# Kernel optimization log

Measured on AMD Instinct MI355X. Metric: run time of the kernel, lower is better.

The kernel has to match this reference:

```python
import jax, jax.numpy as jnp
from jax import lax
import numpy as np

NH = 4                      # num_heads in CrossScaleCom
KS = [3, 5, 7, 9]           # per-head depthwise kernel sizes
WS = 2                      # window_size in LocalFeatureGuided
GGM_K = 7                   # guide-token generator kernel size


def _dwconv(x, w, stride, pad):
    # depthwise conv: w has shape (C, 1, k, k), feature_group_count = C
    return lax.conv_general_dilated(
        x, w, (stride, stride), [(pad, pad), (pad, pad)],
        feature_group_count=x.shape[1],
        dimension_numbers=("NCHW", "OIHW", "NCHW"))


def _forward(x, dw_w0, dw_b0, dw_w1, dw_b1, dw_w2, dw_b2, dw_w3, dw_b3,
             csc_w, csc_b, bn_gamma, bn_beta, bn_mean, bn_var,
             ggm_w, ggm_b, qkv_w, qkv_b, proj_w, proj_b):
    B, C, H, W = x.shape
    cph = C // NH
    # ---- CrossScaleCom: per-head multi-scale depthwise convs ----
    xh = x.reshape(B, NH, cph, H, W)
    dws = [(dw_w0, dw_b0), (dw_w1, dw_b1), (dw_w2, dw_b2), (dw_w3, dw_b3)]
    heads = [_dwconv(xh[:, i], w, 1, KS[i] // 2) + b[None, :, None, None]
             for i, (w, b) in enumerate(dws)]
    y = jnp.stack(heads, 1)                      # (B, NH, cph, H, W)
    y = y.transpose(0, 2, 1, 3, 4).reshape(B, C, H, W)  # channel shuffle
    y = jnp.einsum("bchw,oc->bohw", y, csc_w) + csc_b[None, :, None, None]
    Co = y.shape[1]
    # ---- LocalFeatureGuided ----
    # ggm: BatchNorm (eval) -> GELU (exact) -> depthwise conv k=7 stride=WS
    inv = bn_gamma / jnp.sqrt(bn_var + 1e-5)
    g = (y - bn_mean[None, :, None, None]) * inv[None, :, None, None] \
        + bn_beta[None, :, None, None]
    g = jax.nn.gelu(g, approximate=False)
    g = _dwconv(g, ggm_w, WS, GGM_K // 2) + ggm_b[None, :, None, None]  # (B,Co,Ho,Wo)
    Ho, Wo = H // WS, W // WS
    L = Ho * Wo
    # unfold(kernel=WS, stride=WS) -> (B, Co, WS*WS, L), torch unfold ordering
    xu = y.reshape(B, Co, Ho, WS, Wo, WS).transpose(0, 1, 3, 5, 2, 4)
    xu = xu.reshape(B, Co, WS * WS, L)
    tokens = jnp.concatenate([g.reshape(B, Co, 1, L), xu], axis=2)  # (B,Co,5,L)
    # 1x1 conv over channel dim == einsum
    qkv = jnp.einsum("bcpl,oc->bopl", tokens, qkv_w) + qkv_b[None, :, None, None]
    q, k, v = jnp.split(qkv, 3, axis=1)          # each (B, Co, 5, L)
    # tiny 5x5 attention per (batch, channel), contracting over windows L
    attn = jnp.einsum("bcpl,bcql->bcpq", q, k) / (Co ** 0.5)
    attn = jax.nn.softmax(attn, axis=-1)
    out = jnp.einsum("bcpq,bcql->bcpl", attn, v)  # (B, Co, 5, L)
    out = out[:, :, 0, :].reshape(B, Co, Ho, Wo)  # guide-token output
    out = jnp.einsum("bchw,oc->bohw", out, proj_w) + proj_b[None, :, None, None]
    return out


def setup_inputs() -> dict:
    key = jax.random.key(0)
    ks = jax.random.split(key, 16)
    B, Cin, Cout, H, W = 8, 64, 128, 224, 224
    cph = Cin // NH
    s = 0.05
    d = {"x": jax.random.normal(ks[0], (B, Cin, H, W), jnp.float32)}
    for i, kk in enumerate(KS):
        d[f"dw_w{i}"] = jax.random.normal(ks[1 + i], (cph, 1, kk, kk), jnp.float32) * s
        d[f"dw_b{i}"] = jnp.zeros((cph,), jnp.float32)
    d["csc_w"] = jax.random.normal(ks[5], (Cout, Cin), jnp.float32) * s
    d["csc_b"] = jnp.zeros((Cout,), jnp.float32)
    d["bn_gamma"] = jnp.ones((Cout,), jnp.float32)
    d["bn_beta"] = jnp.zeros((Cout,), jnp.float32)
    d["bn_mean"] = jnp.zeros((Cout,), jnp.float32)
    d["bn_var"] = jnp.ones((Cout,), jnp.float32)
    d["ggm_w"] = jax.random.normal(ks[6], (Cout, 1, GGM_K, GGM_K), jnp.float32) * s
    d["ggm_b"] = jnp.zeros((Cout,), jnp.float32)
    d["qkv_w"] = jax.random.normal(ks[7], (3 * Cout, Cout), jnp.float32) * s
    d["qkv_b"] = jnp.zeros((3 * Cout,), jnp.float32)
    d["proj_w"] = jax.random.normal(ks[8], (Cout, Cout), jnp.float32) * s
    d["proj_b"] = jnp.zeros((Cout,), jnp.float32)
    return d


def reference(x, dw_w0, dw_b0, dw_w1, dw_b1, dw_w2, dw_b2, dw_w3, dw_b3,
              csc_w, csc_b, bn_gamma, bn_beta, bn_mean, bn_var,
              ggm_w, ggm_b, qkv_w, qkv_b, proj_w, proj_b):
    return _forward(x, dw_w0, dw_b0, dw_w1, dw_b1, dw_w2, dw_b2, dw_w3, dw_b3,
                    csc_w, csc_b, bn_gamma, bn_beta, bn_mean, bn_var,
                    ggm_w, ggm_b, qkv_w, qkv_b, proj_w, proj_b)
```

## Files before the change

### kernel.cpp

```cpp
#include <hip/hip_runtime.h>

#define BB 8
#define CIN 64
#define CO 128
#define Hdim 224
#define Wdim 224
#define HWt (224*224)
#define HO 112
#define WO 112
#define Lt (112*112)

typedef unsigned short u16;
typedef short bf16x8 __attribute__((ext_vector_type(8)));
typedef float f32x4  __attribute__((ext_vector_type(4)));
#define MFMA16(a,b,c) __builtin_amdgcn_mfma_f32_16x16x32_bf16((a),(b),(c),0,0,0)

__device__ inline u16 f2bf(float f) {
    union { float f; unsigned u; } v; v.f = f;
    unsigned r = (v.u + 0x7fffu + ((v.u >> 16) & 1u)) >> 16;
    return (u16)r;
}
__device__ inline float bf2f(u16 h) {
    union { unsigned u; float f; } v; v.u = ((unsigned)h) << 16; return v.f;
}
__device__ inline float uasf(unsigned u) {
    union { unsigned u; float f; } v; v.u = u; return v.f;
}
__device__ inline float sum8bf(uint4 v) {
    return bf2f(v.x & 0xffff) + bf2f(v.x >> 16) + bf2f(v.y & 0xffff) + bf2f(v.y >> 16)
         + bf2f(v.z & 0xffff) + bf2f(v.z >> 16) + bf2f(v.w & 0xffff) + bf2f(v.w >> 16);
}

__device__ inline float gelu_fast(float x) {
    float z  = x * 0.7071067811865476f;
    float az = fabsf(z);
    float t  = __builtin_amdgcn_rcpf(fmaf(0.3275911f, az, 1.0f));
    float p  = fmaf(fmaf(fmaf(fmaf(1.061405429f, t, -1.453152027f), t,
                    1.421413741f), t, -0.284496736f), t, 0.254829592f);
    float e  = __expf(-z * z);
    float er = copysignf(1.0f - p * t * e, z);
    return 0.5f * x * (1.0f + er);
}

__global__ void zero_kernel(float* __restrict__ p, int n4) {
    int i = blockIdx.x * 256 + threadIdx.x;
    if (i < n4) ((float4*)p)[i] = make_float4(0.f, 0.f, 0.f, 0.f);
}

template<int HEAD>
__global__ __launch_bounds__(256) void dw_conv(
    const float* __restrict__ x, const float* __restrict__ w,
    const float* __restrict__ bias, u16* __restrict__ dwb)
{
    constexpr int K   = 3 + 2*HEAD;
    constexpr int PAD = HEAD + 1;
    constexpr int R   = 32 + 2*PAD;
    const int tile = blockIdx.x;
    const int c    = blockIdx.y;
    const int b    = blockIdx.z;
    const int th = (tile/7)*32, tw = (tile%7)*32;
    __shared__ float patch[R*40];
    const int tid = threadIdx.x;
    const float* xin = x + (size_t)(b*CIN + HEAD*16 + c)*HWt;
    for (int idx = tid; idx < R*40; idx += 256) {
        int r = idx / 40, cc = idx - r*40;
        int gy = th - PAD + r, gx = tw - 4 + cc;
        float v = 0.f;
        if (gy >= 0 && gy < Hdim && gx >= 0 && gx < Wdim) v = xin[gy*Wdim + gx];
        patch[idx] = v;
    }
    float wreg[K*K];
    const float* wp = w + c*K*K;
    #pragma unroll
    for (int i = 0; i < K*K; i++) wreg[i] = wp[i];
    const float bv = bias[c];
    __syncthreads();

    const int ty = tid >> 3, x0 = (tid & 7) * 4;
    float acc[4] = {bv, bv, bv, bv};
    #pragma unroll
    for (int ky = 0; ky < K; ky++) {
        float rr[12];
        *(float4*)&rr[0] = *(const float4*)&patch[(ty+ky)*40 + x0];
        *(float4*)&rr[4] = *(const float4*)&patch[(ty+ky)*40 + x0 + 4];
        *(float4*)&rr[8] = *(const float4*)&patch[(ty+ky)*40 + x0 + 8];
        #pragma unroll
        for (int kx = 0; kx < K; kx++) {
            const float wv = wreg[ky*K + kx];
            #pragma unroll
            for (int j = 0; j < 4; j++)
                acc[j] = fmaf(rr[j + kx + 4 - PAD], wv, acc[j]);
        }
    }
    const int s = c*4 + HEAD;
    u16 o4[4] = {f2bf(acc[0]), f2bf(acc[1]), f2bf(acc[2]), f2bf(acc[3])};
    *(uint2*)&dwb[(size_t)(b*CIN + s)*HWt + (th+ty)*Wdim + tw + x0] = *(uint2*)o4;
}

__global__ __launch_bounds__(256) void csc_mfma(
    const float* __restrict__ W, const float* __restrict__ bias,
    const u16* __restrict__ dwb, u16* __restrict__ y4)
{
    const int b  = blockIdx.z;
    const int p0 = blockIdx.x * 128;
    __shared__ u16 Abuf[128*72];
    __shared__ u16 Tbuf[32*132];
    const int tid = threadIdx.x;
    const int wv = tid >> 6, ln = tid & 63;
    const int mh = (wv >> 1)*64, nh = (wv & 1)*64;
    const int lm = ln & 15, kq = ln >> 4;
    for (int t = tid; t < 1024; t += 256) {
        int r = t >> 3, kk = (t & 7)*8;
        const float* src = &W[r*64 + kk];
        float4 f0 = *(const float4*)src, f1 = *(const float4*)(src+4);
        u16 tmp[8] = {f2bf(f0.x),f2bf(f0.y),f2bf(f0.z),f2bf(f0.w),
                      f2bf(f1.x),f2bf(f1.y),f2bf(f1.z),f2bf(f1.w)};
        *(uint4*)&Abuf[r*72 + kk] = *(uint4*)tmp;
    }
    const u16* Db = dwb + (size_t)b*CIN*HWt;
    f32x4 acc[4][4];
    #pragma unroll
    for (int i=0;i<4;i++)
        #pragma unroll
        for (int j=0;j<4;j++) acc[i][j] = (f32x4){0.f,0.f,0.f,0.f};

    for (int kc = 0; kc < 64; kc += 32) {
        __syncthreads();
        for (int t = tid; t < 512; t += 256) {
            int k = t >> 4, n0 = (t & 15)*8;
            *(uint4*)&Tbuf[k*132 + n0] = *(const uint4*)&Db[(size_t)(kc+k)*HWt + p0 + n0];
        }
        __syncthreads();
        bf16x8 af[4], bfr[4];
        #pragma unroll
        for (int tm=0;tm<4;tm++)
            af[tm] = *(bf16x8*)&Abuf[(mh + tm*16 + lm)*72 + kc + kq*8];
        #pragma unroll
        for (int tn=0;tn<4;tn++) {
            int n = nh + tn*16 + lm;
            #pragma unroll
            for (int j=0;j<8;j++) bfr[tn][j] = (short)Tbuf[(kq*8+j)*132 + n];
        }
        #pragma unroll
        for (int tm=0;tm<4;tm++)
            #pragma unroll
            for (int tn=0;tn<4;tn++)
                acc[tm][tn] = MFMA16(af[tm], bfr[tn], acc[tm][tn]);
    }
    #pragma unroll
    for (int tm=0;tm<4;tm++) {
        #pragma unroll
        for (int r=0;r<4;r++) {
            int o = mh + tm*16 + kq*4 + r;
            float bb = bias[o];
            #pragma unroll
            for (int tn=0;tn<4;tn++) {
                int p = p0 + nh + tn*16 + lm;
                int gy = p / 224, gx = p - gy*224;
                int w = (gy&1)*2 + (gx&1);
                y4[((size_t)(b*CO + o)*4 + w)*Lt + (gy>>1)*WO + (gx>>1)]
                    = f2bf(acc[tm][tn][r] + bb);
            }
        }
    }
}

__global__ __launch_bounds__(256) void ggm_kernel(const u16* __restrict__ y4,
    const float* __restrict__ gamma, const float* __restrict__ beta,
    const float* __restrict__ mean, const float* __restrict__ var,
    const float* __restrict__ gw, const float* __restrict__ gb,
    u16* __restrict__ gbf)
{
    const int ho0 = blockIdx.x * 16;
    const int c   = blockIdx.y;
    const int b   = blockIdx.z;
    __shared__ float patch[37*272];
    const int tid = threadIdx.x;

    const float inv = gamma[c] * rsqrtf(var[c] + 1e-5f);
    const float bsh = fmaf(-mean[c], inv, beta[c]);
    const u16* ybc = y4 + (size_t)(b*CO + c)*4*Lt;

    for (int idx = tid; idx < 37*14; idx += 256) {
        int r = idx / 14, q = idx - r*14;
        int gy = 2*ho0 - 3 + r;
        float* dst = &patch[r*272 + 4*((r>>1)&7) + 8 + 16*q];
        if (gy >= 0 && gy < Hdim) {
            const u16* pe = ybc + (size_t)((gy&1)*2)*Lt + (gy>>1)*WO + 8*q;
            uint4 ve = *(const uint4*)pe;
            uint4 vo = *(const uint4*)(pe + Lt);
            unsigned eu[4] = {ve.x, ve.y, ve.z, ve.w};
            unsigned ou[4] = {vo.x, vo.y, vo.z, vo.w};
            float o[16];
            #pragma unroll
            for (int i = 0; i < 4; i++) {
                float e0 = uasf(eu[i] << 16), e1 = uasf(eu[i] & 0xffff0000u);
                float d0 = uasf(ou[i] << 16), d1 = uasf(ou[i] & 0xffff0000u);
                o[4*i+0] = gelu_fast(fmaf(e0, inv, bsh));
                o[4*i+1] = gelu_fast(fmaf(d0, inv, bsh));
                o[4*i+2] = gelu_fast(fmaf(e1, inv, bsh));
                o[4*i+3] = gelu_fast(fmaf(d1, inv, bsh));
            }
            #pragma unroll
            for (int i = 0; i < 4; i++)
                *(float4*)&dst[4*i] = *(float4*)&o[4*i];
        } else {
            float4 z = make_float4(0.f,0.f,0.f,0.f);
            #pragma unroll
            for (int i = 0; i < 4; i++) *(float4*)&dst[4*i] = z;
        }
    }
    for (int idx = tid; idx < 37*2; idx += 256) {
        int r = idx >> 1, side = idx & 1;
        float* dst = &patch[r*272 + 4*((r>>1)&7) + (side ? 232 : 0)];
        float4 z = make_float4(0.f,0.f,0.f,0.f);
        *(float4*)&dst[0] = z; *(float4*)&dst[4] = z;
    }
    float wk[49];
    const float* wp = gw + c*49;
    #pragma unroll
    for (int i = 0; i < 49; i++) wk[i] = wp[i];
    const float bv = gb[c];
    __syncthreads();

    const int ty = tid >> 4, m = tid & 15;
    if (m < 14) {
        float acc[8] = {bv,bv,bv,bv,bv,bv,bv,bv};
        #pragma unroll
        for (int ky = 0; ky < 7; ky++) {
            int r = 2*ty + ky;
            const float* row = &patch[r*272 + 4*((r>>1)&7) + 16*m + 4];
            float f[24];
            #pragma unroll
            for (int u = 0; u < 6; u++)
                *(float4*)&f[4*u] = *(const float4*)&row[4*u];
            #pragma unroll
            for (int kx = 0; kx < 7; kx++) {
                const float wv = wk[ky*7 + kx];
                #pragma unroll
                for (int j = 0; j < 8; j++)
                    acc[j] = fmaf(f[2*j + kx + 1], wv, acc[j]);
            }
        }
        u16 o8[8];
        #pragma unroll
        for (int j = 0; j < 8; j++) o8[j] = f2bf(acc[j]);
        *(uint4*)&gbf[(size_t)(b*CO + c)*Lt + (ho0 + ty)*WO + 8*m] = *(uint4*)o8;
    }
}

__global__ __launch_bounds__(256) void G_mfma(
    const u16* __restrict__ gbf, const u16* __restrict__ y4,
    float* __restrict__ G)
{
    const int b = blockIdx.z, p = blockIdx.y, split = blockIdx.x;
    const u16* Ab = gbf + (size_t)b*CO*Lt;
    const u16* Bb; int brs;
    if (p == 0) { Bb = Ab; brs = Lt; }
    else        { Bb = y4 + ((size_t)b*CO*4 + (p-1))*Lt; brs = 4*Lt; }
    __shared__ u16 Abuf[128*40];
    __shared__ u16 Bbuf[128*40];
    const int tid = threadIdx.x;
    const int wv = tid >> 6, ln = tid & 63;
    const int mh = (wv >> 1)*64, nh = (wv & 1)*64;
    const int lm = ln & 15, kq = ln >> 4;
    f32x4 acc[4][4];
    #pragma unroll
    for (int i=0;i<4;i++)
        #pragma unroll
        for (int j=0;j<4;j++) acc[i][j] = (f32x4){0.f,0.f,0.f,0.f};

    for (int ci = split; ci < 392; ci += 32) {
        const int l0 = ci*32;
        __syncthreads();
        for (int t = tid; t < 512; t += 256) {
            int r = t >> 2, kk = (t & 3)*8;
            *(uint4*)&Abuf[r*40 + kk] = *(const uint4*)&Ab[(size_t)r*Lt  + l0 + kk];
            *(uint4*)&Bbuf[r*40 + kk] = *(const uint4*)&Bb[(size_t)r*brs + l0 + kk];
        }
        __syncthreads();
        bf16x8 af[4], bfr[4];
        #pragma unroll
        for (int tm=0;tm<4;tm++)
            af[tm]  = *(bf16x8*)&Abuf[(mh + tm*16 + lm)*40 + kq*8];
        #pragma unroll
        for (int tn=0;tn<4;tn++)
            bfr[tn] = *(bf16x8*)&Bbuf[(nh + tn*16 + lm)*40 + kq*8];
        #pragma unroll
        for (int tm=0;tm<4;tm++)
            #pragma unroll
            for (int tn=0;tn<4;tn++)
                acc[tm][tn] = MFMA16(af[tm], bfr[tn], acc[tm][tn]);
    }
    float* Go = G + ((size_t)(b*5 + p))*CO*CO;
    #pragma unroll
    for (int tm=0;tm<4;tm++)
        #pragma unroll
        for (int r=0;r<4;r++) {
            int mrow = mh + tm*16 + kq*4 + r;
            #pragma unroll
            for (int tn=0;tn<4;tn++)
                atomicAdd(&Go[mrow*CO + nh + tn*16 + lm], acc[tm][tn][r]);
        }
}

__global__ void S_kernel(const u16* __restrict__ gbf, const u16* __restrict__ y4,
                         float* __restrict__ S)
{
    const int b = blockIdx.x >> 7, c = blockIdx.x & 127;
    const u16* gr = gbf + (size_t)(b*CO+c)*Lt;
    const u16* yr = y4  + (size_t)(b*CO+c)*4*Lt;
    float vals[5] = {0.f,0.f,0.f,0.f,0.f};
    for (int i = threadIdx.x*8; i < Lt; i += 256*8)
        vals[0] += sum8bf(*(const uint4*)&gr[i]);
    #pragma unroll
    for (int w=0; w<4; w++)
        for (int i = threadIdx.x*8; i < Lt; i += 256*8)
            vals[1+w] += sum8bf(*(const uint4*)&yr[(size_t)w*Lt + i]);
    #pragma unroll
    for (int off=32; off>0; off>>=1) {
        #pragma unroll
        for (int q=0;q<5;q++) vals[q] += __shfl_down(vals[q], off);
    }
    __shared__ float red[4][5];
    const int wid = threadIdx.x>>6, lane = threadIdx.x&63;
    if (lane==0) {
        #pragma unroll
        for (int q=0;q<5;q++) red[wid][q] = vals[q];
    }
    __syncthreads();
    if (threadIdx.x==0) {
        #pragma unroll
        for (int q=0;q<5;q++)
            S[((size_t)b*5 + q)*CO + c] = red[0][q]+red[1][q]+red[2][q]+red[3][q];
    }
}

__global__ __launch_bounds__(256) void fused_logits_kernel(
    const float* __restrict__ G, const float* __restrict__ S,
    const float* __restrict__ qkv_w, const float* __restrict__ qkv_b,
    float* __restrict__ lg)
{
    const int p = blockIdx.x, b = blockIdx.y;
    __shared__ float Wl[32*132];
    __shared__ float Al[32*132];
    __shared__ float KGl[128*128];
    const int tid = threadIdx.x;
    const int og = (tid >> 4) * 8;
    const int pg = (tid & 15) * 8;
    const float* Gp = G + (size_t)(b*5 + p)*CO*CO;
    float acc[8][8];
    #pragma unroll
    for (int i=0;i<8;i++)
        #pragma unroll
        for (int j=0;j<8;j++) acc[i][j]=0.f;

    for (int kc = 0; kc < 128; kc += 32) {
        __syncthreads();
        for (int t = tid; t < 4096; t += 256) {
            int kk = t & 31, o = t >> 5;
            Wl[kk*132 + o] = Gp[(size_t)o*CO + kc + kk];
            Al[kk*132 + o] = qkv_w[(size_t)(CO + o)*CO + kc + kk];
        }
        __syncthreads();
        #pragma unroll 4
        for (int kk = 0; kk < 32; kk++) {
            float wv[8], av[8];
            *(float4*)&wv[0] = *(const float4*)&Wl[kk*132+og];
            *(float4*)&wv[4] = *(const float4*)&Wl[kk*132+og+4];
            *(float4*)&av[0] = *(const float4*)&Al[kk*132+pg];
            *(float4*)&av[4] = *(const float4*)&Al[kk*132+pg+4];
            #pragma unroll
            for (int i=0;i<8;i++)
                #pragma unroll
                for (int j=0;j<8;j++)
                    acc[i][j] = fmaf(wv[i], av[j], acc[i][j]);
        }
    }
    #pragma unroll
    for (int i=0;i<8;i++) {
        #pragma unroll
        for (int j=0;j<8;j+=4)
            *(float4*)&KGl[(og+i)*128 + pg + j] = *(float4*)&acc[i][j];
    }
    __syncthreads();
    if (tid < 128) {
        const int c = tid;
        const float qb = qkv_b[c], kb = qkv_b[CO + c];
        const float* S0 = S + (size_t)b*5*CO;
        const float* Sp = S0 + p*CO;
        const float* qwrow = qkv_w + (size_t)c*CO;
        const float* kwrow = qkv_w + (size_t)(CO + c)*CO;
        float sq = qb * 12544.f, ks = 0.f, s = 0.f;
        for (int c2 = 0; c2 < CO; c2++) {
            sq = fmaf(qwrow[c2], S0[c2], sq);
            ks = fmaf(kwrow[c2], Sp[c2], ks);
            s  = fmaf(qwrow[c2], KGl[c2*128 + c], s);
        }
        lg[(size_t)(b*5 + p)*CO + c] = s + qb*ks + kb*sq;
    }
}

__global__ void softmax5_kernel(const float* __restrict__ lg, float* __restrict__ a)
{
    const int b = blockIdx.x, c = threadIdx.x;
    float v[5];
    #pragma unroll
    for (int p=0;p<5;p++) v[p] = lg[(size_t)(b*5 + p)*CO + c];
    const float scl = 0.08838834764831845f;
    float mx = v[0];
    #pragma unroll
    for (int p=1;p<5;p++) mx = fmaxf(mx, v[p]);
    float e[5], sum = 0.f;
    #pragma unroll
    for (int p=0;p<5;p++){ e[p] = __expf((v[p]-mx)*scl); sum += e[p]; }
    const float rs = 1.f/sum;
    #pragma unroll
    for (int p=0;p<5;p++) a[((size_t)b*CO + c)*5 + p] = e[p]*rs;
}

__global__ void F_kernel(const float* __restrict__ proj_w,
    const float* __restrict__ qkv_w, const float* __restrict__ a,
    float* __restrict__ F)
{
    const int b = blockIdx.z, p = blockIdx.y;
    const int o  = blockIdx.x*2 + (threadIdx.x>>7);
    const int cp = threadIdx.x & 127;
    const float* vw = qkv_w + 2*CO*CO;
    float s = 0.f;
    for (int c=0;c<CO;c++)
        s = fmaf(proj_w[o*CO+c] * a[((size_t)b*CO+c)*5 + p], vw[c*CO+cp], s);
    F[(((size_t)(b*5+p))*CO + o)*CO + cp] = s;
}

__global__ void bias_kernel(const float* __restrict__ proj_w,
    const float* __restrict__ proj_b, const float* __restrict__ qkv_b,
    float* __restrict__ biasout)
{
    const int o = threadIdx.x;
    const float* vb = qkv_b + 2*CO;
    float s = proj_b[o];
    for (int c=0;c<CO;c++) s = fmaf(proj_w[o*CO+c], vb[c], s);
    biasout[o] = s;
}

__global__ __launch_bounds__(256) void final_mfma(
    const float* __restrict__ F, const u16* __restrict__ gbf,
    const u16* __restrict__ y4, const float* __restrict__ biasout,
    float* __restrict__ out)
{
    const int b = blockIdx.z;
    const int p0 = blockIdx.x * 128;
    __shared__ u16 Abuf[128*40];
    __shared__ u16 Tbuf[32*132];
    const int tid = threadIdx.x;
    const int wv = tid >> 6, ln = tid & 63;
    const int mh = (wv >> 1)*64, nh = (wv & 1)*64;
    const int lm = ln & 15, kq = ln >> 4;
    f32x4 acc[4][4];
    #pragma unroll
    for (int i=0;i<4;i++)
        #pragma unroll
        for (int j=0;j<4;j++) acc[i][j] = (f32x4){0.f,0.f,0.f,0.f};

    for (int ph = 0; ph < 5; ph++) {
        const float* Fp = F + (size_t)(b*5 + ph)*CO*CO;
        const u16* Bb; int brs;
        if (ph == 0) { Bb = gbf + (size_t)b*CO*Lt; brs = Lt; }
        else         { Bb = y4 + ((size_t)b*CO*4 + (ph-1))*Lt; brs = 4*Lt; }
        for (int kc = 0; kc < CO; kc += 32) {
            __syncthreads();
            for (int t = tid; t < 512; t += 256) {
                int r = t >> 2, kk = (t & 3)*8;
                const float* src = &Fp[r*CO + kc + kk];
                float4 f0 = *(const float4*)src, f1 = *(const float4*)(src+4);
                u16 tmp[8] = {f2bf(f0.x),f2bf(f0.y),f2bf(f0.z),f2bf(f0.w),
                              f2bf(f1.x),f2bf(f1.y),f2bf(f1.z),f2bf(f1.w)};
                *(uint4*)&Abuf[r*40 + kk] = *(uint4*)tmp;
            }
            for (int t = tid; t < 512; t += 256) {
                int k = t >> 4, n0 = (t & 15)*8;
                *(uint4*)&Tbuf[k*132 + n0] = *(const uint4*)&Bb[(size_t)(kc+k)*brs + p0 + n0];
            }
            __syncthreads();
            bf16x8 af[4], bfr[4];
            #pragma unroll
            for (int tm=0;tm<4;tm++)
                af[tm] = *(bf16x8*)&Abuf[(mh + tm*16 + lm)*40 + kq*8];
            #pragma unroll
            for (int tn=0;tn<4;tn++) {
                int n = nh + tn*16 + lm;
                #pragma unroll
                for (int j=0;j<8;j++) bfr[tn][j] = (short)Tbuf[(kq*8+j)*132 + n];
            }
            #pragma unroll
            for (int tm=0;tm<4;tm++)
                #pragma unroll
                for (int tn=0;tn<4;tn++)
                    acc[tm][tn] = MFMA16(af[tm], bfr[tn], acc[tm][tn]);
        }
    }
    float* Ob = out + (size_t)b*CO*Lt;
    #pragma unroll
    for (int tm=0;tm<4;tm++) {
        #pragma unroll
        for (int r=0;r<4;r++) {
            int o = mh + tm*16 + kq*4 + r;
            float bb = biasout[o];
            #pragma unroll
            for (int tn=0;tn<4;tn++)
                Ob[(size_t)o*Lt + p0 + nh + tn*16 + lm] = acc[tm][tn][r] + bb;
        }
    }
}

extern "C" void kernel_launch(void* const* d_in, const int* in_sizes, int n_in,
                              void* d_out, int out_size, void* d_ws, size_t ws_size,
                              hipStream_t stream) {
    const float* x      = (const float*)d_in[0];
    const float* dw_w0  = (const float*)d_in[1];
    const float* dw_b0  = (const float*)d_in[2];
    const float* dw_w1  = (const float*)d_in[3];
    const float* dw_b1  = (const float*)d_in[4];
    const float* dw_w2  = (const float*)d_in[5];
    const float* dw_b2  = (const float*)d_in[6];
    const float* dw_w3  = (const float*)d_in[7];
    const float* dw_b3  = (const float*)d_in[8];
    const float* csc_w  = (const float*)d_in[9];
    const float* csc_b  = (const float*)d_in[10];
    const float* bn_g   = (const float*)d_in[11];
    const float* bn_b   = (const float*)d_in[12];
    const float* bn_m   = (const float*)d_in[13];
    const float* bn_v   = (const float*)d_in[14];
    const float* ggm_w  = (const float*)d_in[15];
    const float* ggm_b  = (const float*)d_in[16];
    const float* qkv_w  = (const float*)d_in[17];
    const float* qkv_b  = (const float*)d_in[18];
    const float* proj_w = (const float*)d_in[19];
    const float* proj_b = (const float*)d_in[20];
    float* out = (float*)d_out;

    char* ws = (char*)d_ws;
    u16*   y4  = (u16*)(ws);
    u16*   dwb = (u16*)(ws + 102760448);
    u16*   gbf = (u16*)(ws + 154140672);
    float* G   = (float*)(ws + 179830784);
    float* lgb = G  + 655360;
    float* F   = lgb + 5120;
    float* S   = F  + 655360;
    float* aw  = S  + 5120;
    float* bo  = aw + 5120;

    zero_kernel<<<dim3(640), 256, 0, stream>>>(G, 655360/4);

    dw_conv<0><<<dim3(49, 16, 8), 256, 0, stream>>>(x, dw_w0, dw_b0, dwb);
    dw_conv<1><<<dim3(49, 16, 8), 256, 0, stream>>>(x, dw_w1, dw_b1, dwb);
    dw_conv<2><<<dim3(49, 16, 8), 256, 0, stream>>>(x, dw_w2, dw_b2, dwb);
    dw_conv<3><<<dim3(49, 16, 8), 256, 0, stream>>>(x, dw_w3, dw_b3, dwb);

    csc_mfma<<<dim3(392, 1, 8), 256, 0, stream>>>(csc_w, csc_b, dwb, y4);

    ggm_kernel<<<dim3(7, 128, 8), 256, 0, stream>>>(
        y4, bn_g, bn_b, bn_m, bn_v, ggm_w, ggm_b, gbf);

    G_mfma<<<dim3(32, 5, 8), 256, 0, stream>>>(gbf, y4, G);

    S_kernel<<<dim3(1024), 256, 0, stream>>>(gbf, y4, S);

    fused_logits_kernel<<<dim3(5, 8), 256, 0, stream>>>(G, S, qkv_w, qkv_b, lgb);

    softmax5_kernel<<<dim3(8), 128, 0, stream>>>(lgb, aw);

    F_kernel<<<dim3(64, 5, 8), 256, 0, stream>>>(proj_w, qkv_w, aw, F);
    bias_kernel<<<dim3(1), 128, 0, stream>>>(proj_w, proj_b, qkv_b, bo);

    final_mfma<<<dim3(98, 1, 8), 256, 0, stream>>>(F, gbf, y4, bo, out);
}
```

Before: 723.9 us.

## Restructure ggm depthwise conv thread mapping to reuse rows across outputs

Result: faster. 693.8 us (-4.2%).

```diff
diff --git a/kernel.cpp b/kernel.cpp
--- a/kernel.cpp
+++ b/kernel.cpp
@@ -174,78 +174,68 @@
     const int ho0 = blockIdx.x * 16;
     const int c   = blockIdx.y;
     const int b   = blockIdx.z;
-    __shared__ float patch[37*272];
+    __shared__ float patch[37*240];
     const int tid = threadIdx.x;
 
     const float inv = gamma[c] * rsqrtf(var[c] + 1e-5f);
     const float bsh = fmaf(-mean[c], inv, beta[c]);
     const u16* ybc = y4 + (size_t)(b*CO + c)*4*Lt;
 
-    for (int idx = tid; idx < 37*14; idx += 256) {
-        int r = idx / 14, q = idx - r*14;
-        int gy = 2*ho0 - 3 + r;
-        float* dst = &patch[r*272 + 4*((r>>1)&7) + 8 + 16*q];
-        if (gy >= 0 && gy < Hdim) {
-            const u16* pe = ybc + (size_t)((gy&1)*2)*Lt + (gy>>1)*WO + 8*q;
-            uint4 ve = *(const uint4*)pe;
-            uint4 vo = *(const uint4*)(pe + Lt);
-            unsigned eu[4] = {ve.x, ve.y, ve.z, ve.w};
-            unsigned ou[4] = {vo.x, vo.y, vo.z, vo.w};
-            float o[16];
-            #pragma unroll
-            for (int i = 0; i < 4; i++) {
-                float e0 = uasf(eu[i] << 16), e1 = uasf(eu[i] & 0xffff0000u);
-                float d0 = uasf(ou[i] << 16), d1 = uasf(ou[i] & 0xffff0000u);
-                o[4*i+0] = gelu_fast(fmaf(e0, inv, bsh));
-                o[4*i+1] = gelu_fast(fmaf(d0, inv, bsh));
-                o[4*i+2] = gelu_fast(fmaf(e1, inv, bsh));
-                o[4*i+3] = gelu_fast(fmaf(d1, inv, bsh));
-            }
-            #pragma unroll
-            for (int i = 0; i < 4; i++)
-                *(float4*)&dst[4*i] = *(float4*)&o[4*i];
-        } else {
-            float4 z = make_float4(0.f,0.f,0.f,0.f);
-            #pragma unroll
-            for (int i = 0; i < 4; i++) *(float4*)&dst[4*i] = z;
-        }
-    }
-    for (int idx = tid; idx < 37*2; idx += 256) {
-        int r = idx >> 1, side = idx & 1;
-        float* dst = &patch[r*272 + 4*((r>>1)&7) + (side ? 232 : 0)];
-        float4 z = make_float4(0.f,0.f,0.f,0.f);
-        *(float4*)&dst[0] = z; *(float4*)&dst[4] = z;
-    }
     float wk[49];
     const float* wp = gw + c*49;
     #pragma unroll
     for (int i = 0; i < 49; i++) wk[i] = wp[i];
     const float bv = gb[c];
+
+    for (int idx = tid; idx < 37*60; idx += 256) {
+        int r = idx / 60, j = idx - r*60;
+        int gy = 2*ho0 - 3 + r;
+        float4 v = make_float4(0.f, 0.f, 0.f, 0.f);
+        if (gy >= 0 && gy < Hdim && j >= 2 && j <= 57) {
+            const u16* pe = ybc + (size_t)((gy&1)*2)*Lt + (gy>>1)*WO + (2*j - 4);
+            unsigned e = *(const unsigned*)pe;
+            unsigned o = *(const unsigned*)(pe + Lt);
+            v.x = gelu_fast(fmaf(uasf(e << 16),         inv, bsh));
+            v.y = gelu_fast(fmaf(uasf(o << 16),         inv, bsh));
+            v.z = gelu_fast(fmaf(uasf(e & 0xffff0000u), inv, bsh));
+            v.w = gelu_fast(fmaf(uasf(o & 0xffff0000u), inv, bsh));
+        }
+        *(float4*)&patch[idx*4] = v;
+    }
     __syncthreads();
 
-    const int ty = tid >> 4, m = tid & 15;
-    if (m < 14) {
-        float acc[8] = {bv,bv,bv,bv,bv,bv,bv,bv};
-        #pragma unroll
-        for (int ky = 0; ky < 7; ky++) {
-            int r = 2*ty + ky;
-            const float* row = &patch[r*272 + 4*((r>>1)&7) + 16*m + 4];
-            float f[24];
-            #pragma unroll
-            for (int u = 0; u < 6; u++)
-                *(float4*)&f[4*u] = *(const float4*)&row[4*u];
-            #pragma unroll
-            for (int kx = 0; kx < 7; kx++) {
-                const float wv = wk[ky*7 + kx];
-                #pragma unroll
-                for (int j = 0; j < 8; j++)
-                    acc[j] = fmaf(f[2*j + kx + 1], wv, acc[j]);
+    if (tid < 224) {
+        const int n = tid % 56;
+        const int g = tid / 56;
+        float acc[4][2];
+        #pragma unroll
+        for (int i = 0; i < 4; i++) { acc[i][0] = bv; acc[i][1] = bv; }
+        #pragma unroll
+        for (int rr = 0; rr < 13; rr++) {
+            const float* row = &patch[(8*g + rr)*240 + 4*n + 4];
+            float f[12];
+            *(float4*)&f[0] = *(const float4*)&row[0];
+            *(float4*)&f[4] = *(const float4*)&row[4];
+            *(float4*)&f[8] = *(const float4*)&row[8];
+            #pragma unroll
+            for (int i = 0; i < 4; i++) {
+                const int ky = rr - 2*i;
+                if (ky >= 0 && ky <= 6) {
+                    #pragma unroll
+                    for (int kx = 0; kx < 7; kx++) {
+                        const float wv = wk[ky*7 + kx];
+                        acc[i][0] = fmaf(f[kx + 1], wv, acc[i][0]);
+                        acc[i][1] = fmaf(f[kx + 3], wv, acc[i][1]);
+                    }
+                }
             }
         }
-        u16 o8[8];
-        #pragma unroll
-        for (int j = 0; j < 8; j++) o8[j] = f2bf(acc[j]);
-        *(uint4*)&gbf[(size_t)(b*CO + c)*Lt + (ho0 + ty)*WO + 8*m] = *(uint4*)o8;
+        u16* gout = gbf + (size_t)(b*CO + c)*Lt;
+        #pragma unroll
+        for (int i = 0; i < 4; i++) {
+            u16 o2[2] = {f2bf(acc[i][0]), f2bf(acc[i][1])};
+            *(unsigned*)&gout[(ho0 + 4*g + i)*WO + 2*n] = *(unsigned*)o2;
+        }
     }
 }
 
```
